# Optimization experiments

Measured on AMD Instinct MI355X. Metric: run time of the kernel, lower is better.

The kernel has to match this reference:

```python
import jax, jax.numpy as jnp
import numpy as np

GAMMA = 2.0  # focal focusing parameter
LAM = 0.1    # disco weight


def _centered_dist(x, nw):
    """Doubly (weighted) centered pairwise |x_i - x_j| matrix, as in distance_corr."""
    d = jnp.abs(x[:, None] - x[None, :])          # [N, N]
    davg = jnp.mean(d * nw, axis=1)               # [N]  (row-wise weighted mean)
    return d - davg[None, :] - davg[:, None] + jnp.mean(davg * nw)


def _dcorr(Amat, Bmat, nw):
    ABavg = jnp.mean(Amat * Bmat * nw, axis=1)
    AAavg = jnp.mean(Amat * Amat * nw, axis=1)
    BBavg = jnp.mean(Bmat * Bmat * nw, axis=1)
    return jnp.mean(ABavg * nw) / jnp.sqrt(jnp.mean(AAavg * nw) * jnp.mean(BBavg * nw))


def setup_inputs() -> dict:
    key = jax.random.key(0)
    k1, k2, k3, k4 = jax.random.split(key, 4)
    N, C = 8192, 4
    return {
        "outputs": jax.random.normal(k1, (N, C), dtype=jnp.float32),
        "labels": jax.random.randint(k2, (N,), 0, C, dtype=jnp.int32),
        "event": jax.random.normal(k3, (N,), dtype=jnp.float32),
        "weights": jax.random.uniform(k4, (N, 1), dtype=jnp.float32, minval=0.1, maxval=1.0),
    }


def reference(outputs, labels, event, weights):
    N, C = outputs.shape
    w = weights.squeeze()                          # [N]

    # Focal loss (reduction='none'), alpha=None
    logp = jax.nn.log_softmax(outputs, axis=1)     # [N, C]
    logpt = logp[jnp.arange(N), labels]            # [N]
    pt = jnp.exp(logpt)
    focal = -(1.0 - pt) ** GAMMA * logpt * w       # per-example, times weights

    probs = jnp.exp(logp)                          # softmax(outputs)
    nw = w * N / jnp.sum(w)                        # normed weights (sum == N)

    # event-side centered distance matrix is class-independent: compute once
    Bmat = _centered_dist(event, nw)               # [N, N]

    disco = jnp.float32(0.0)
    for i in range(C):                             # small fixed class loop
        Amat = _centered_dist(probs[:, i], nw)
        disco = disco + _dcorr(Amat, Bmat, nw)
    disco = disco / C

    f = jnp.mean(focal)
    return jnp.stack([f, disco, f + LAM * disco])  # [focal, disco, tot]
```

## Files before the change

### kernel.cpp

```cpp
#include <hip/hip_runtime.h>
#include <math.h>

#define BLK 256
#define IT 4
#define JSP 128
#define LAM 0.1f


__device__ __forceinline__ float wave_reduce(float v) {
    v += __shfl_down(v, 32, 64);
    v += __shfl_down(v, 16, 64);
    v += __shfl_down(v, 8, 64);
    v += __shfl_down(v, 4, 64);
    v += __shfl_down(v, 2, 64);
    v += __shfl_down(v, 1, 64);
    return v;
}

__global__ __launch_bounds__(BLK) void fused_pairs(
        const float4* __restrict__ outs4, const int* __restrict__ labels,
        const float* __restrict__ event, const float* __restrict__ wts,
        float* __restrict__ rows, float* __restrict__ scal,
        float* __restrict__ out, int N) {
    __shared__ float4 jp[64];
    __shared__ float2 jew[64];
    __shared__ float redm[4][12];
    __shared__ float red[4][14];
    __shared__ int lastFlag;

    int tid = threadIdx.x;
    int itile = blockIdx.x;
    int jsp = blockIdx.y;
    int lane = tid & 63, wave = tid >> 6;
    int ibase = itile * (BLK * IT) + tid;

    float4 pi[IT];
    float ei[IT], wi[IT];
    float vals[12];
    if (jsp == 0) {
#pragma unroll
        for (int k = 0; k < 12; ++k) vals[k] = 0.f;
    }
#pragma unroll
    for (int k = 0; k < IT; ++k) {
        int i = ibase + k * BLK;
        float4 o = outs4[i];
        float m = fmaxf(fmaxf(o.x, o.y), fmaxf(o.z, o.w));
        float e0 = expf(o.x - m), e1 = expf(o.y - m),
              e2 = expf(o.z - m), e3 = expf(o.w - m);
        float inv = 1.0f / (e0 + e1 + e2 + e3);
        pi[k] = make_float4(e0 * inv, e1 * inv, e2 * inv, e3 * inv);
        ei[k] = event[i];
        wi[k] = wts[i];
        if (jsp == 0) {
            int l = labels[i];
            float pl = (l == 0) ? pi[k].x : (l == 1) ? pi[k].y
                     : (l == 2) ? pi[k].z : pi[k].w;
            float logpt = logf(pl);
            float om = 1.0f - pl;
            float w = wi[k];
            vals[0] += -om * om * logpt * w;
            vals[1] += w;
            vals[2] += w * pi[k].x;
            vals[3] += w * pi[k].y;
            vals[4] += w * pi[k].z;
            vals[5] += w * pi[k].w;
            vals[6] += w * ei[k];
            vals[7] += w * pi[k].x * pi[k].x;
            vals[8] += w * pi[k].y * pi[k].y;
            vals[9] += w * pi[k].z * pi[k].z;
            vals[10] += w * pi[k].w * pi[k].w;
            vals[11] += w * ei[k] * ei[k];
        }
    }

    if (tid < 64) {
        int j = jsp * 64 + tid;
        float4 o = outs4[j];
        float m = fmaxf(fmaxf(o.x, o.y), fmaxf(o.z, o.w));
        float e0 = expf(o.x - m), e1 = expf(o.y - m),
              e2 = expf(o.z - m), e3 = expf(o.w - m);
        float inv = 1.0f / (e0 + e1 + e2 + e3);
        jp[tid] = make_float4(e0 * inv, e1 * inv, e2 * inv, e3 * inv);
        jew[tid] = make_float2(event[j], wts[j]);
    }
    if (jsp == 0) {
#pragma unroll
        for (int k = 0; k < 12; ++k) {
            float r = wave_reduce(vals[k]);
            if (lane == 0) redm[wave][k] = r;
        }
    }
    __syncthreads();
    if (jsp == 0 && tid < 12)
        atomicAdd(&scal[4 + tid],
                  redm[0][tid] + redm[1][tid] + redm[2][tid] + redm[3][tid]);

    float s[IT][5], t[IT][4];
#pragma unroll
    for (int k = 0; k < IT; ++k) {
#pragma unroll
        for (int v = 0; v < 5; ++v) s[k][v] = 0.f;
#pragma unroll
        for (int v = 0; v < 4; ++v) t[k][v] = 0.f;
    }

#pragma unroll 16
    for (int jj = 0; jj < 64; ++jj) {
        float4 p = jp[jj];
        float2 ew = jew[jj];
        float wj = ew.y;
#pragma unroll
        for (int k = 0; k < IT; ++k) {
            float d0 = pi[k].x - p.x;
            float d1 = pi[k].y - p.y;
            float d2 = pi[k].z - p.z;
            float d3 = pi[k].w - p.w;
            float de = ei[k] - ew.x;
            s[k][0] = fmaf(wj, fabsf(d0), s[k][0]);
            s[k][1] = fmaf(wj, fabsf(d1), s[k][1]);
            s[k][2] = fmaf(wj, fabsf(d2), s[k][2]);
            s[k][3] = fmaf(wj, fabsf(d3), s[k][3]);
            float wde = wj * fabsf(de);
            s[k][4] += wde;
            t[k][0] = fmaf(wde, fabsf(d0), t[k][0]);
            t[k][1] = fmaf(wde, fabsf(d1), t[k][1]);
            t[k][2] = fmaf(wde, fabsf(d2), t[k][2]);
            t[k][3] = fmaf(wde, fabsf(d3), t[k][3]);
        }
    }

#pragma unroll
    for (int k = 0; k < IT; ++k) {
        int i = ibase + k * BLK;
        atomicAdd(&rows[0 * N + i], s[k][0]);
        atomicAdd(&rows[1 * N + i], s[k][1]);
        atomicAdd(&rows[2 * N + i], s[k][2]);
        atomicAdd(&rows[3 * N + i], s[k][3]);
        atomicAdd(&rows[4 * N + i], s[k][4]);
    }

    float tc0 = t[0][0] * wi[0] + t[1][0] * wi[1] + t[2][0] * wi[2] + t[3][0] * wi[3];
    float tc1 = t[0][1] * wi[0] + t[1][1] * wi[1] + t[2][1] * wi[2] + t[3][1] * wi[3];
    float tc2 = t[0][2] * wi[0] + t[1][2] * wi[1] + t[2][2] * wi[2] + t[3][2] * wi[3];
    float tc3 = t[0][3] * wi[0] + t[1][3] * wi[1] + t[2][3] * wi[2] + t[3][3] * wi[3];
    tc0 = wave_reduce(tc0); tc1 = wave_reduce(tc1);
    tc2 = wave_reduce(tc2); tc3 = wave_reduce(tc3);
    if (lane == 0) {
        red[wave][0] = tc0; red[wave][1] = tc1;
        red[wave][2] = tc2; red[wave][3] = tc3;
    }
    __syncthreads();
    if (tid < 4)
        atomicAdd(&scal[tid], red[0][tid] + red[1][tid] + red[2][tid] + red[3][tid]);

    __syncthreads();
    if (tid == 0) {
        __threadfence();
        float old = atomicAdd(&scal[16], 1.0f);
        float total = (float)(gridDim.x * gridDim.y);
        lastFlag = (old > total - 1.5f) ? 1 : 0;
    }
    __syncthreads();

    if (lastFlag) {
        __threadfence();

        float acc[14];
#pragma unroll
        for (int k = 0; k < 14; ++k) acc[k] = 0.f;

        const float4* w4 = (const float4*)wts;
        const float4* r0 = (const float4*)(rows + 0 * N);
        const float4* r1 = (const float4*)(rows + 1 * N);
        const float4* r2 = (const float4*)(rows + 2 * N);
        const float4* r3 = (const float4*)(rows + 3 * N);
        const float4* r4 = (const float4*)(rows + 4 * N);

        for (int q = tid; q < N / 4; q += BLK) {
            float4 ww = w4[q];
            float4 a0 = r0[q], a1 = r1[q], a2 = r2[q], a3 = r3[q], aE = r4[q];
#define DO_COMP(c)                                                        \
            {                                                             \
                float w_ = ww.c;                                          \
                float s0 = a0.c, s1 = a1.c, s2 = a2.c, s3 = a3.c,         \
                      sE = aE.c;                                          \
                acc[0] += w_ * s0; acc[1] += w_ * s1; acc[2] += w_ * s2;  \
                acc[3] += w_ * s3; acc[4] += w_ * sE;                     \
                float wE = w_ * sE;                                       \
                acc[5] += wE * s0; acc[6] += wE * s1;                     \
                acc[7] += wE * s2; acc[8] += wE * s3;                     \
                acc[9] += wE * sE;                                        \
                acc[10] += w_ * s0 * s0; acc[11] += w_ * s1 * s1;         \
                acc[12] += w_ * s2 * s2; acc[13] += w_ * s3 * s3;         \
            }
            DO_COMP(x) DO_COMP(y) DO_COMP(z) DO_COMP(w)
#undef DO_COMP
        }

#pragma unroll
        for (int k = 0; k < 14; ++k) acc[k] = wave_reduce(acc[k]);
        __syncthreads();
        if (lane == 0) {
#pragma unroll
            for (int k = 0; k < 14; ++k) red[wave][k] = acc[k];
        }
        __syncthreads();

        if (tid == 0) {
            float SW[5], SWW_ce[4], SWW_ee, SWW_cc[4];
#pragma unroll
            for (int k = 0; k < 5; ++k)
                SW[k] = red[0][k] + red[1][k] + red[2][k] + red[3][k];
#pragma unroll
            for (int k = 0; k < 4; ++k)
                SWW_ce[k] = red[0][5 + k] + red[1][5 + k] + red[2][5 + k] + red[3][5 + k];
            SWW_ee = red[0][9] + red[1][9] + red[2][9] + red[3][9];
#pragma unroll
            for (int k = 0; k < 4; ++k)
                SWW_cc[k] = red[0][10 + k] + red[1][10 + k] + red[2][10 + k] + red[3][10 + k];

            float focal_sum = scal[4];
            float W = scal[5];
            float M1[5] = {scal[6], scal[7], scal[8], scal[9], scal[10]};
            float M2[5] = {scal[11], scal[12], scal[13], scal[14], scal[15]};

            float invW2 = 1.0f / (W * W);
            float invW3 = invW2 / W;

            float g[5];
#pragma unroll
            for (int v = 0; v < 5; ++v) g[v] = SW[v] * invW2;
            float gE = g[4];

            float Tee = 2.0f * (W * M2[4] - M1[4] * M1[4]);
            float num_ee = Tee * invW2 - 2.0f * SWW_ee * invW3 + gE * gE;

            float disco = 0.f;
#pragma unroll
            for (int c = 0; c < 4; ++c) {
                float Tcc = 2.0f * (W * M2[c] - M1[c] * M1[c]);
                float num_cc = Tcc * invW2 - 2.0f * SWW_cc[c] * invW3 + g[c] * g[c];
                float num_ce = scal[c] * invW2 - 2.0f * SWW_ce[c] * invW3 + g[c] * gE;
                disco += num_ce * rsqrtf(num_cc * num_ee);
            }
            disco *= 0.25f;

            float f = focal_sum / (float)N;
            out[0] = f;
            out[1] = disco;
            out[2] = f + LAM * disco;
        }
    }
}

extern "C" void kernel_launch(void* const* d_in, const int* in_sizes, int n_in,
                              void* d_out, int out_size, void* d_ws, size_t ws_size,
                              hipStream_t stream) {
    const float4* outs4 = (const float4*)d_in[0];
    const int* labels = (const int*)d_in[1];
    const float* event = (const float*)d_in[2];
    const float* wts = (const float*)d_in[3];
    float* out = (float*)d_out;
    int N = in_sizes[1];

    float* ws = (float*)d_ws;
    float* rows = ws;
    float* scal = rows + (size_t)N * 5;

    dim3 g(N / (BLK * IT), JSP);
    fused_pairs<<<g, BLK, 0, stream>>>(outs4, labels, event, wts, rows, scal, out, N);
}
```

Baseline: 110.5 us.

## Replace per-row global atomics with partial buffers and a separate reduction kernel

The pairwise kernel now writes per-j-slice partial row sums into a dedicated workspace slab instead of atomically adding them into shared row arrays. A second kernel sums the slices per row, forms the weighted moments, and finishes the loss with a last-block step. The serial single-block tail is removed. The j-slice count is halved, so each block processes 128 j-points. In exchange, several megabytes of partials are written and read back, a second launch is added, and the pair kernel has half as many blocks.

```diff
diff --git a/kernel.cpp b/kernel.cpp
--- a/kernel.cpp
+++ b/kernel.cpp
@@ -3,7 +3,7 @@
 
 #define BLK 256
 #define IT 4
-#define JSP 128
+#define JSP 64
 #define LAM 0.1f
 
 
@@ -17,22 +17,21 @@
     return v;
 }
 
-__global__ __launch_bounds__(BLK) void fused_pairs(
+__global__ __launch_bounds__(BLK) void kA_pairs(
         const float4* __restrict__ outs4, const int* __restrict__ labels,
         const float* __restrict__ event, const float* __restrict__ wts,
-        float* __restrict__ rows, float* __restrict__ scal,
-        float* __restrict__ out, int N) {
-    __shared__ float4 jp[64];
-    __shared__ float2 jew[64];
+        float* __restrict__ part, float* __restrict__ scal, int N) {
+    __shared__ float4 jp[128];
+    __shared__ float2 jew[128];
     __shared__ float redm[4][12];
-    __shared__ float red[4][14];
-    __shared__ int lastFlag;
+    __shared__ float red[4][4];
 
     int tid = threadIdx.x;
     int itile = blockIdx.x;
     int jsp = blockIdx.y;
     int lane = tid & 63, wave = tid >> 6;
     int ibase = itile * (BLK * IT) + tid;
+    int jbase = jsp * (N / JSP);
 
     float4 pi[IT];
     float ei[IT], wi[IT];
@@ -74,8 +73,8 @@
         }
     }
 
-    if (tid < 64) {
-        int j = jsp * 64 + tid;
+    if (tid < 128) {
+        int j = jbase + tid;
         float4 o = outs4[j];
         float m = fmaxf(fmaxf(o.x, o.y), fmaxf(o.z, o.w));
         float e0 = expf(o.x - m), e1 = expf(o.y - m),
@@ -105,8 +104,8 @@
         for (int v = 0; v < 4; ++v) t[k][v] = 0.f;
     }
 
-#pragma unroll 16
-    for (int jj = 0; jj < 64; ++jj) {
+#pragma unroll 8
+    for (int jj = 0; jj < 128; ++jj) {
         float4 p = jp[jj];
         float2 ew = jew[jj];
         float wj = ew.y;
@@ -133,11 +132,9 @@
 #pragma unroll
     for (int k = 0; k < IT; ++k) {
         int i = ibase + k * BLK;
-        atomicAdd(&rows[0 * N + i], s[k][0]);
-        atomicAdd(&rows[1 * N + i], s[k][1]);
-        atomicAdd(&rows[2 * N + i], s[k][2]);
-        atomicAdd(&rows[3 * N + i], s[k][3]);
-        atomicAdd(&rows[4 * N + i], s[k][4]);
+#pragma unroll
+        for (int v = 0; v < 5; ++v)
+            part[((size_t)(v * JSP + jsp)) * N + i] = s[k][v];
     }
 
     float tc0 = t[0][0] * wi[0] + t[1][0] * wi[1] + t[2][0] * wi[2] + t[3][0] * wi[3];
@@ -153,104 +150,92 @@
     __syncthreads();
     if (tid < 4)
         atomicAdd(&scal[tid], red[0][tid] + red[1][tid] + red[2][tid] + red[3][tid]);
+}
+
+__global__ __launch_bounds__(BLK) void kB_final(
+        const float* __restrict__ part, const float* __restrict__ wts,
+        float* __restrict__ scal, float* __restrict__ out, int N) {
+    __shared__ float red[4][14];
+    __shared__ int lastFlag;
+    int tid = threadIdx.x, lane = tid & 63, wave = tid >> 6;
+    int i = blockIdx.x * BLK + tid;
+
+    float sv[5];
+#pragma unroll
+    for (int v = 0; v < 5; ++v) {
+        float a = 0.f;
+        const float* p = part + ((size_t)(v * JSP)) * N + i;
+#pragma unroll 8
+        for (int jsp = 0; jsp < JSP; ++jsp) a += p[(size_t)jsp * N];
+        sv[v] = a;
+    }
+
+    float w = wts[i];
+    float wE = w * sv[4];
+    float acc[14] = {w * sv[0], w * sv[1], w * sv[2], w * sv[3], w * sv[4],
+                     wE * sv[0], wE * sv[1], wE * sv[2], wE * sv[3], wE * sv[4],
+                     w * sv[0] * sv[0], w * sv[1] * sv[1],
+                     w * sv[2] * sv[2], w * sv[3] * sv[3]};
+#pragma unroll
+    for (int k = 0; k < 14; ++k) acc[k] = wave_reduce(acc[k]);
+    if (lane == 0) {
+#pragma unroll
+        for (int k = 0; k < 14; ++k) red[wave][k] = acc[k];
+    }
+    __syncthreads();
+    if (tid < 14)
+        atomicAdd(&scal[17 + tid],
+                  red[0][tid] + red[1][tid] + red[2][tid] + red[3][tid]);
 
     __syncthreads();
     if (tid == 0) {
         __threadfence();
         float old = atomicAdd(&scal[16], 1.0f);
-        float total = (float)(gridDim.x * gridDim.y);
-        lastFlag = (old > total - 1.5f) ? 1 : 0;
-    }
-    __syncthreads();
-
-    if (lastFlag) {
+        lastFlag = (old > (float)gridDim.x - 1.5f) ? 1 : 0;
+    }
+    __syncthreads();
+
+    if (lastFlag && tid == 0) {
         __threadfence();
-
-        float acc[14];
-#pragma unroll
-        for (int k = 0; k < 14; ++k) acc[k] = 0.f;
-
-        const float4* w4 = (const float4*)wts;
-        const float4* r0 = (const float4*)(rows + 0 * N);
-        const float4* r1 = (const float4*)(rows + 1 * N);
-        const float4* r2 = (const float4*)(rows + 2 * N);
-        const float4* r3 = (const float4*)(rows + 3 * N);
-        const float4* r4 = (const float4*)(rows + 4 * N);
-
-        for (int q = tid; q < N / 4; q += BLK) {
-            float4 ww = w4[q];
-            float4 a0 = r0[q], a1 = r1[q], a2 = r2[q], a3 = r3[q], aE = r4[q];
-#define DO_COMP(c)                                                        \
-            {                                                             \
-                float w_ = ww.c;                                          \
-                float s0 = a0.c, s1 = a1.c, s2 = a2.c, s3 = a3.c,         \
-                      sE = aE.c;                                          \
-                acc[0] += w_ * s0; acc[1] += w_ * s1; acc[2] += w_ * s2;  \
-                acc[3] += w_ * s3; acc[4] += w_ * sE;                     \
-                float wE = w_ * sE;                                       \
-                acc[5] += wE * s0; acc[6] += wE * s1;                     \
-                acc[7] += wE * s2; acc[8] += wE * s3;                     \
-                acc[9] += wE * sE;                                        \
-                acc[10] += w_ * s0 * s0; acc[11] += w_ * s1 * s1;         \
-                acc[12] += w_ * s2 * s2; acc[13] += w_ * s3 * s3;         \
-            }
-            DO_COMP(x) DO_COMP(y) DO_COMP(z) DO_COMP(w)
-#undef DO_COMP
-        }
-
-#pragma unroll
-        for (int k = 0; k < 14; ++k) acc[k] = wave_reduce(acc[k]);
-        __syncthreads();
-        if (lane == 0) {
-#pragma unroll
-            for (int k = 0; k < 14; ++k) red[wave][k] = acc[k];
-        }
-        __syncthreads();
-
-        if (tid == 0) {
-            float SW[5], SWW_ce[4], SWW_ee, SWW_cc[4];
-#pragma unroll
-            for (int k = 0; k < 5; ++k)
-                SW[k] = red[0][k] + red[1][k] + red[2][k] + red[3][k];
-#pragma unroll
-            for (int k = 0; k < 4; ++k)
-                SWW_ce[k] = red[0][5 + k] + red[1][5 + k] + red[2][5 + k] + red[3][5 + k];
-            SWW_ee = red[0][9] + red[1][9] + red[2][9] + red[3][9];
-#pragma unroll
-            for (int k = 0; k < 4; ++k)
-                SWW_cc[k] = red[0][10 + k] + red[1][10 + k] + red[2][10 + k] + red[3][10 + k];
-
-            float focal_sum = scal[4];
-            float W = scal[5];
-            float M1[5] = {scal[6], scal[7], scal[8], scal[9], scal[10]};
-            float M2[5] = {scal[11], scal[12], scal[13], scal[14], scal[15]};
-
-            float invW2 = 1.0f / (W * W);
-            float invW3 = invW2 / W;
-
-            float g[5];
-#pragma unroll
-            for (int v = 0; v < 5; ++v) g[v] = SW[v] * invW2;
-            float gE = g[4];
-
-            float Tee = 2.0f * (W * M2[4] - M1[4] * M1[4]);
-            float num_ee = Tee * invW2 - 2.0f * SWW_ee * invW3 + gE * gE;
-
-            float disco = 0.f;
-#pragma unroll
-            for (int c = 0; c < 4; ++c) {
-                float Tcc = 2.0f * (W * M2[c] - M1[c] * M1[c]);
-                float num_cc = Tcc * invW2 - 2.0f * SWW_cc[c] * invW3 + g[c] * g[c];
-                float num_ce = scal[c] * invW2 - 2.0f * SWW_ce[c] * invW3 + g[c] * gE;
-                disco += num_ce * rsqrtf(num_cc * num_ee);
-            }
-            disco *= 0.25f;
-
-            float f = focal_sum / (float)N;
-            out[0] = f;
-            out[1] = disco;
-            out[2] = f + LAM * disco;
-        }
+        float SW[5], SWW_ce[4], SWW_ee, SWW_cc[4];
+#pragma unroll
+        for (int k = 0; k < 5; ++k) SW[k] = scal[17 + k];
+#pragma unroll
+        for (int k = 0; k < 4; ++k) SWW_ce[k] = scal[22 + k];
+        SWW_ee = scal[26];
+#pragma unroll
+        for (int k = 0; k < 4; ++k) SWW_cc[k] = scal[27 + k];
+
+        float focal_sum = scal[4];
+        float W = scal[5];
+        float M1[5] = {scal[6], scal[7], scal[8], scal[9], scal[10]};
+        float M2[5] = {scal[11], scal[12], scal[13], scal[14], scal[15]};
+
+        float invW2 = 1.0f / (W * W);
+        float invW3 = invW2 / W;
+
+        float g[5];
+#pragma unroll
+        for (int v = 0; v < 5; ++v) g[v] = SW[v] * invW2;
+        float gE = g[4];
+
+        float Tee = 2.0f * (W * M2[4] - M1[4] * M1[4]);
+        float num_ee = Tee * invW2 - 2.0f * SWW_ee * invW3 + gE * gE;
+
+        float disco = 0.f;
+#pragma unroll
+        for (int c = 0; c < 4; ++c) {
+            float Tcc = 2.0f * (W * M2[c] - M1[c] * M1[c]);
+            float num_cc = Tcc * invW2 - 2.0f * SWW_cc[c] * invW3 + g[c] * g[c];
+            float num_ce = scal[c] * invW2 - 2.0f * SWW_ce[c] * invW3 + g[c] * gE;
+            disco += num_ce * rsqrtf(num_cc * num_ee);
+        }
+        disco *= 0.25f;
+
+        float f = focal_sum / (float)N;
+        out[0] = f;
+        out[1] = disco;
+        out[2] = f + LAM * disco;
     }
 }
 
@@ -265,9 +250,11 @@
     int N = in_sizes[1];
 
     float* ws = (float*)d_ws;
-    float* rows = ws;
-    float* scal = rows + (size_t)N * 5;
-
-    dim3 g(N / (BLK * IT), JSP);
-    fused_pairs<<<g, BLK, 0, stream>>>(outs4, labels, event, wts, rows, scal, out, N);
-}
+    float* part = ws;
+    float* scal = part + (size_t)5 * JSP * N;
+
+    dim3 gA(N / (BLK * IT), JSP);
+    kA_pairs<<<gA, BLK, 0, stream>>>(outs4, labels, event, wts, part, scal, N);
+
+    kB_final<<<N / BLK, BLK, 0, stream>>>(part, wts, scal, out, N);
+}
```

Result: faster. 108.1 us (-2.2%).
